# Kernel tuning notes

Hardware: AMD Instinct MI355X
Metric: run time of the kernel (lower is better)

Reference implementation:

```python
import jax, jax.numpy as jnp
import numpy as np

EPS = 1e-5

def _bn(x, g, b):
    # eval-mode BatchNorm2d with running_mean=0, running_var=1
    return x * (g / jnp.sqrt(1.0 + EPS))[None, :, None, None] + b[None, :, None, None]

def _dwconv2d(x, w, kh, kw, ph, pw):
    C = x.shape[1]
    k = w.reshape(C, 1, kh, kw)
    return jax.lax.conv_general_dilated(x, k, (1, 1), [(ph, ph), (pw, pw)],
                                        dimension_numbers=('NCHW', 'OIHW', 'NCHW'),
                                        feature_group_count=C)

def _mamba_seq(x, ln_g, ln_b, in_w, conv_w, conv_b, xproj_w, dt_w, dt_b, A_log, Dp, out_w):
    # x: (B, L, C) -> LayerNorm -> Mamba block (mamba-ssm math)
    B, L, C = x.shape
    di = conv_w.shape[0]; ds = A_log.shape[1]; dtr = dt_w.shape[1]; dc = conv_w.shape[1]
    mu = x.mean(-1, keepdims=True)
    var = ((x - mu) ** 2).mean(-1, keepdims=True)
    xn = (x - mu) / jnp.sqrt(var + EPS) * ln_g + ln_b
    xz = xn @ in_w.T                      # (B, L, 2*di)
    xm, z = xz[..., :di], xz[..., di:]
    # causal depthwise conv1d along L
    xc = xm.transpose(0, 2, 1)            # (B, di, L)
    k = conv_w.reshape(di, 1, dc)
    xc = jax.lax.conv_general_dilated(xc, k, (1,), [(dc - 1, 0)],
                                      dimension_numbers=('NCH', 'OIH', 'NCH'),
                                      feature_group_count=di)
    xm = jax.nn.silu((xc + conv_b[None, :, None]).transpose(0, 2, 1))  # (B, L, di)
    proj = xm @ xproj_w.T                 # (B, L, dtr + 2*ds)
    dt = jax.nn.softplus(proj[..., :dtr] @ dt_w.T + dt_b)              # (B, L, di)
    Bm = proj[..., dtr:dtr + ds]          # (B, L, ds)
    Cm = proj[..., dtr + ds:]             # (B, L, ds)
    A = -jnp.exp(A_log)                   # (di, ds)
    dA = jnp.exp(dt[..., None] * A)                       # (B, L, di, ds)
    dBx = (dt * xm)[..., None] * Bm[:, :, None, :]        # (B, L, di, ds)

    def step(h, inp):
        dA_t, dBx_t, C_t = inp
        h = dA_t * h + dBx_t
        y = jnp.einsum('bds,bs->bd', h, C_t)
        return h, y

    h0 = jnp.zeros((B, di, ds), x.dtype)
    xs = (dA.transpose(1, 0, 2, 3), dBx.transpose(1, 0, 2, 3), Cm.transpose(1, 0, 2))
    _, ys = jax.lax.scan(step, h0, xs)
    y = ys.transpose(1, 0, 2) + Dp * xm
    y = y * jax.nn.silu(z)
    return y @ out_w.T

def _mamba2d(x, *mp):
    B, C, H, W = x.shape
    s = x.reshape(B, C, H * W).transpose(0, 2, 1)
    s = _mamba_seq(s, *mp)
    return s.transpose(0, 2, 1).reshape(B, C, H, W)

def _forward(x, reduce_w, bn0_g, bn0_b, proj_w, bn1_g, bn1_b, dwh_w, bnh_g, bnh_b,
             dwv_w, bnv_g, bnv_b, fus_w, fus_b, ln_g, ln_b, in_w, conv_w, conv_b,
             xproj_w, dt_w, dt_b, A_log, Dp, out_w, fc1_w, fc2_w):
    C = reduce_w.shape[0]
    x = jax.nn.relu(_bn(jnp.einsum('bchw,oc->bohw', x, reduce_w), bn0_g, bn0_b))
    # local branch: StripConvBlock (depthwise strips)
    p = jax.nn.relu(_bn(jnp.einsum('bchw,oc->bohw', x, proj_w), bn1_g, bn1_b))
    h = jax.nn.relu(_bn(_dwconv2d(p, dwh_w, 1, 7, 0, 3), bnh_g, bnh_b))
    v = jax.nn.relu(_bn(_dwconv2d(p, dwv_w, 7, 1, 3, 0), bnv_g, bnv_b))
    feat_local = jnp.einsum('bchw,oc->bohw', h + v, fus_w) + fus_b[None, :, None, None]
    # global branch: 4-directional shared-weight Mamba
    mp = (ln_g, ln_b, in_w, conv_w, conv_b, xproj_w, dt_w, dt_b, A_log, Dp, out_w)
    x1 = _mamba2d(x, *mp)
    x2 = _mamba2d(x[:, :, ::-1, ::-1], *mp)[:, :, ::-1, ::-1]
    xt = x.swapaxes(2, 3)
    x3 = _mamba2d(xt, *mp).swapaxes(2, 3)
    x4 = _mamba2d(xt[:, :, ::-1, ::-1], *mp)[:, :, ::-1, ::-1].swapaxes(2, 3)
    feat_global = (x1 + x2 + x3 + x4) / 4.0 + x
    # SK fusion
    U = feat_local + feat_global
    s = U.mean((2, 3))                                   # (B, C)
    zf = jax.nn.relu(s @ fc1_w.T) @ fc2_w.T              # (B, 2C)
    w = jax.nn.softmax(zf.reshape(-1, 2, C), axis=1)
    return w[:, 0, :, None, None] * feat_local + w[:, 1, :, None, None] * feat_global

def setup_inputs() -> dict:
    key = jax.random.key(0)
    ks = jax.random.split(key, 16)
    B, Cin, C, H, W = 2, 512, 256, 48, 48
    di, ds, dtr, dc, mid = 512, 16, 16, 4, 16
    n = lambda i, shape, s=0.05: jax.random.normal(ks[i], shape, jnp.float32) * s
    return {
        'x': n(0, (B, Cin, H, W), 1.0),
        'reduce_w': n(1, (C, Cin)),
        'bn0_g': jnp.ones(C), 'bn0_b': jnp.zeros(C),
        'proj_w': n(2, (C, C)),
        'bn1_g': jnp.ones(C), 'bn1_b': jnp.zeros(C),
        'dwh_w': n(3, (C, 7), 0.2), 'bnh_g': jnp.ones(C), 'bnh_b': jnp.zeros(C),
        'dwv_w': n(4, (C, 7), 0.2), 'bnv_g': jnp.ones(C), 'bnv_b': jnp.zeros(C),
        'fus_w': n(5, (C, C)), 'fus_b': jnp.zeros(C),
        'ln_g': jnp.ones(C), 'ln_b': jnp.zeros(C),
        'in_w': n(6, (2 * di, C)),
        'conv_w': n(7, (di, dc), 0.2), 'conv_b': jnp.zeros(di),
        'xproj_w': n(8, (dtr + 2 * ds, di)),
        'dt_w': n(9, (di, dtr)), 'dt_b': jnp.full((di,), -4.0, jnp.float32),
        'A_log': jnp.tile(jnp.log(jnp.arange(1, ds + 1, dtype=jnp.float32)), (di, 1)),
        'Dp': jnp.ones(di),
        'out_w': n(10, (C, di)),
        'fc1_w': n(11, (mid, C)), 'fc2_w': n(12, (2 * C, mid)),
    }

def reference(x, reduce_w, bn0_g, bn0_b, proj_w, bn1_g, bn1_b, dwh_w, bnh_g, bnh_b,
              dwv_w, bnv_g, bnv_b, fus_w, fus_b, ln_g, ln_b, in_w, conv_w, conv_b,
              xproj_w, dt_w, dt_b, A_log, Dp, out_w, fc1_w, fc2_w):
    return _forward(x, reduce_w, bn0_g, bn0_b, proj_w, bn1_g, bn1_b, dwh_w, bnh_g, bnh_b,
                    dwv_w, bnv_g, bnv_b, fus_w, fus_b, ln_g, ln_b, in_w, conv_w, conv_b,
                    xproj_w, dt_w, dt_b, A_log, Dp, out_w, fc1_w, fc2_w)
```

## Files before the change

kernel.cpp:

```cpp
#include <hip/hip_runtime.h>
#include <hip/hip_bf16.h>

#define EPSC 1e-5f
#define Bn 2
#define CIN 512
#define Cc 256
#define Hh 48
#define Ww 48
#define Ll 2304
#define DI 512
#define DS 16
#define DTR 16
#define MROWS (Bn * Ll)
#define NCHUNK 8
#define CLEN (Ll / NCHUNK)
#define CTILES (CLEN / 32)

using bf16 = __hip_bfloat16;
typedef short v8s __attribute__((ext_vector_type(8)));
typedef float v4f __attribute__((ext_vector_type(4)));

__device__ __forceinline__ float ldIn(const void* p, size_t i, bool bf) {
    return bf ? __bfloat162float(((const bf16*)p)[i]) : ((const float*)p)[i];
}
__device__ __forceinline__ float toF(float v) { return v; }
__device__ __forceinline__ float toF(bf16 v) { return __bfloat162float(v); }
__device__ __forceinline__ void stO(float* p, float v) { *p = v; }
__device__ __forceinline__ void stO(bf16* p, float v) { *p = __float2bfloat16(v); }
__device__ __forceinline__ float bfu2f(unsigned short u) {
    return __uint_as_float(((unsigned int)u) << 16);
}
__device__ __forceinline__ short f2bs(float f) {
    bf16 h = __float2bfloat16(f);
    short s;
    __builtin_memcpy(&s, &h, 2);
    return s;
}
union U16B { uint4 u; v8s v; };
__device__ __forceinline__ v8s ldA8(const bf16* p) { U16B t; t.u = *(const uint4*)p; return t.v; }
__device__ __forceinline__ v8s ldW8(const void* W, size_t idx, bool bf) {
    if (bf) return ldA8((const bf16*)W + idx);
    const float* f = (const float*)W + idx;
    float4 a = *(const float4*)f;
    float4 b = *(const float4*)(f + 4);
    v8s r;
    r[0] = f2bs(a.x); r[1] = f2bs(a.y); r[2] = f2bs(a.z); r[3] = f2bs(a.w);
    r[4] = f2bs(b.x); r[5] = f2bs(b.y); r[6] = f2bs(b.z); r[7] = f2bs(b.w);
    return r;
}

__device__ __forceinline__ int perm_rt(int dir, int t) {
    if (dir == 0) return t;
    if (dir == 1) return Ll - 1 - t;
    int tt = (dir == 2) ? t : (Ll - 1 - t);
    int h = tt % Hh, w = tt / Hh;
    return h * Ww + w;
}

__global__ void k_detect(const unsigned int* __restrict__ xb, int* __restrict__ flag) {
    if (threadIdx.x == 0 && blockIdx.x == 0) {
        int cnt = 0;
        for (int i = 0; i < 64; i++) {
            unsigned int u = xb[i];
            unsigned int lo = u & 0xFFFFu;
            int e = (int)((lo >> 7) & 0xFF);
            if (lo == 0u || (e >= 90 && e <= 160)) cnt++;
        }
        *flag = (cnt >= 60) ? 1 : 0;
    }
}

__global__ __launch_bounds__(256) void k_probe(bf16* __restrict__ out, int n, float val) {
    int i = blockIdx.x * 256 + threadIdx.x;
    if (i < n) out[i] = __float2bfloat16(val);
}

__global__ __launch_bounds__(256) void k_transpose_in(const void* __restrict__ x, bf16* __restrict__ xT,
                                                      const int* __restrict__ dflag) {
    bool bf = (*dflag != 0);
    __shared__ float tile[32][33];
    int b = blockIdx.z;
    int l0 = blockIdx.x * 32, c0 = blockIdx.y * 32;
    int tx = threadIdx.x, ty = threadIdx.y;
    #pragma unroll
    for (int i = 0; i < 4; i++) {
        int c = c0 + ty + i * 8;
        tile[ty + i * 8][tx] = ldIn(x, ((size_t)(b * CIN + c)) * Ll + l0 + tx, bf);
    }
    __syncthreads();
    #pragma unroll
    for (int i = 0; i < 4; i++) {
        int l = l0 + ty + i * 8;
        xT[((size_t)(b * Ll + l)) * CIN + c0 + tx] = __float2bfloat16(tile[tx][ty + i * 8]);
    }
}

template <int EP, int KT, typename TO>
__global__ __launch_bounds__(256) void k_mgemm(const bf16* __restrict__ A, const void* __restrict__ W,
                                               TO* __restrict__ Out, int M, int N,
                                               const void* __restrict__ g, const void* __restrict__ bias,
                                               const int* __restrict__ dflag) {
    bool bf = (*dflag != 0);
    constexpr int K = KT * 32;
    int tid = threadIdx.x;
    int w = tid >> 6, lane = tid & 63, quad = lane >> 4, lm = lane & 15;
    int m_w = blockIdx.y * 128 + w * 32;
    int n_w = blockIdx.x * 64;
    v4f acc[2][4] = {};
    const bf16* aP0 = A + (size_t)(m_w + lm) * K + quad * 8;
    const bf16* aP1 = A + (size_t)(m_w + 16 + lm) * K + quad * 8;
    size_t wIdx[4];
    #pragma unroll
    for (int ni = 0; ni < 4; ni++) {
        int n = n_w + ni * 16 + lm;
        wIdx[ni] = (size_t)((n < N) ? n : 0) * K + quad * 8;
    }
    for (int kt = 0; kt < KT; kt++) {
        v8s a0 = ldA8(aP0 + kt * 32);
        v8s a1 = ldA8(aP1 + kt * 32);
        v8s bfr[4];
        #pragma unroll
        for (int ni = 0; ni < 4; ni++) bfr[ni] = ldW8(W, wIdx[ni] + kt * 32, bf);
        #pragma unroll
        for (int ni = 0; ni < 4; ni++) {
            acc[0][ni] = __builtin_amdgcn_mfma_f32_16x16x32_bf16(a0, bfr[ni], acc[0][ni], 0, 0, 0);
            acc[1][ni] = __builtin_amdgcn_mfma_f32_16x16x32_bf16(a1, bfr[ni], acc[1][ni], 0, 0, 0);
        }
    }
    float rs = rsqrtf(1.f + EPSC);
    #pragma unroll
    for (int mi = 0; mi < 2; mi++) {
        #pragma unroll
        for (int ni = 0; ni < 4; ni++) {
            int col = n_w + ni * 16 + lm;
            if (col >= N) continue;
            float gv = 0.f, bv = 0.f;
            if (EP == 1) { gv = ldIn(g, col, bf) * rs; bv = ldIn(bias, col, bf); }
            if (EP == 2) { bv = ldIn(bias, col, bf); }
            #pragma unroll
            for (int r = 0; r < 4; r++) {
                int row = m_w + mi * 16 + quad * 4 + r;
                float v = acc[mi][ni][r];
                if (EP == 1) v = fmaxf(v * gv + bv, 0.f);
                else if (EP == 2) v += bv;
                stO(&Out[(size_t)row * N + col], v);
            }
        }
    }
}

__global__ __launch_bounds__(256) void k_outgemm(const bf16* __restrict__ Y, const void* __restrict__ W,
                                                 const bf16* __restrict__ xrb, float* __restrict__ fg,
                                                 const int* __restrict__ dflag) {
    bool bf = (*dflag != 0);
    int tid = threadIdx.x;
    int w = tid >> 6, lane = tid & 63, quad = lane >> 4, lm = lane & 15;
    int row0 = blockIdx.y * 128 + w * 32;
    int n_w = blockIdx.x * 64;
    int b = row0 / Ll;
    v4f acc[2][4] = {};
    const bf16* aP[4][2];
    #pragma unroll
    for (int mi = 0; mi < 2; mi++) {
        int l = (row0 + mi * 16 + lm) - b * Ll;
        int h = l / Ww, w2 = l % Ww;
        int t2 = w2 * Hh + h;
        int tArr[4] = { l, Ll - 1 - l, t2, Ll - 1 - t2 };
        #pragma unroll
        for (int dir = 0; dir < 4; dir++)
            aP[dir][mi] = Y + ((size_t)dir * MROWS + (size_t)b * Ll + tArr[dir]) * DI + quad * 8;
    }
    size_t wIdx[4];
    #pragma unroll
    for (int ni = 0; ni < 4; ni++) wIdx[ni] = (size_t)(n_w + ni * 16 + lm) * DI + quad * 8;
    for (int kt = 0; kt < 16; kt++) {
        v8s bfr[4];
        #pragma unroll
        for (int ni = 0; ni < 4; ni++) bfr[ni] = ldW8(W, wIdx[ni] + kt * 32, bf);
        #pragma unroll
        for (int dir = 0; dir < 4; dir++) {
            v8s a0 = ldA8(aP[dir][0] + kt * 32);
            v8s a1 = ldA8(aP[dir][1] + kt * 32);
            #pragma unroll
            for (int ni = 0; ni < 4; ni++) {
                acc[0][ni] = __builtin_amdgcn_mfma_f32_16x16x32_bf16(a0, bfr[ni], acc[0][ni], 0, 0, 0);
                acc[1][ni] = __builtin_amdgcn_mfma_f32_16x16x32_bf16(a1, bfr[ni], acc[1][ni], 0, 0, 0);
            }
        }
    }
    #pragma unroll
    for (int mi = 0; mi < 2; mi++) {
        #pragma unroll
        for (int ni = 0; ni < 4; ni++) {
            int col = n_w + ni * 16 + lm;
            #pragma unroll
            for (int r = 0; r < 4; r++) {
                int row = row0 + mi * 16 + quad * 4 + r;
                size_t off = (size_t)row * Cc + col;
                fg[off] = toF(xrb[off]) + 0.25f * acc[mi][ni][r];
            }
        }
    }
}

__global__ __launch_bounds__(256) void k_ln(const bf16* __restrict__ xrb, const void* __restrict__ g,
                                            const void* __restrict__ bvec, bf16* __restrict__ xn,
                                            const int* __restrict__ dflag) {
    bool bf = (*dflag != 0);
    int m = blockIdx.x;
    int c = threadIdx.x;
    float v = toF(xrb[(size_t)m * Cc + c]);
    float s1 = v, s2 = v * v;
    #pragma unroll
    for (int off = 32; off; off >>= 1) {
        s1 += __shfl_down(s1, off);
        s2 += __shfl_down(s2, off);
    }
    __shared__ float a1[4], a2[4];
    int w = c >> 6;
    if ((c & 63) == 0) { a1[w] = s1; a2[w] = s2; }
    __syncthreads();
    float t1 = a1[0] + a1[1] + a1[2] + a1[3];
    float t2 = a2[0] + a2[1] + a2[2] + a2[3];
    float mu = t1 * (1.f / 256.f);
    float var = t2 * (1.f / 256.f) - mu * mu;
    float r = rsqrtf(var + EPSC);
    xn[(size_t)m * Cc + c] = __float2bfloat16((v - mu) * r * ldIn(g, c, bf) + ldIn(bvec, c, bf));
}

__global__ __launch_bounds__(256) void k_dwconv_hv(const bf16* __restrict__ p, const void* __restrict__ dwh,
                                                   const void* __restrict__ bnhg, const void* __restrict__ bnhb,
                                                   const void* __restrict__ dwv, const void* __restrict__ bnvg,
                                                   const void* __restrict__ bnvb, bf16* __restrict__ hv,
                                                   const int* __restrict__ dflag) {
    bool bf = (*dflag != 0);
    int m = blockIdx.x;
    int c = threadIdx.x;
    int b = m / Ll, l = m % Ll;
    int yy = l / Ww, xx = l % Ww;
    const bf16* base = p + (size_t)b * Ll * Cc;
    float ah = 0.f, av = 0.f;
    #pragma unroll
    for (int j = 0; j < 7; j++) {
        int x2 = xx + j - 3;
        if (0 <= x2 && x2 < Ww) ah += ldIn(dwh, c * 7 + j, bf) * toF(base[(size_t)(yy * Ww + x2) * Cc + c]);
        int y2 = yy + j - 3;
        if (0 <= y2 && y2 < Hh) av += ldIn(dwv, c * 7 + j, bf) * toF(base[(size_t)(y2 * Ww + xx) * Cc + c]);
    }
    float rs = rsqrtf(1.f + EPSC);
    float out = fmaxf(ah * ldIn(bnhg, c, bf) * rs + ldIn(bnhb, c, bf), 0.f) +
                fmaxf(av * ldIn(bnvg, c, bf) * rs + ldIn(bnvb, c, bf), 0.f);
    hv[(size_t)m * Cc + c] = __float2bfloat16(out);
}

__global__ __launch_bounds__(512) void k_conv1d(const bf16* __restrict__ xz, const void* __restrict__ cw,
                                                const void* __restrict__ cb, bf16* __restrict__ xm2,
                                                const int* __restrict__ dflag) {
    bool bf = (*dflag != 0);
    int m = blockIdx.x;
    int dir = blockIdx.y;
    int ch = threadIdx.x;
    int b = m / Ll, t = m % Ll;
    float acc = ldIn(cb, ch, bf);
    #pragma unroll
    for (int j = 0; j < 4; j++) {
        int tt = t + j - 3;
        if (tt >= 0) {
            int l = perm_rt(dir, tt);
            acc += ldIn(cw, ch * 4 + j, bf) * __bfloat162float(xz[((size_t)(b * Ll + l)) * 1024 + ch]);
        }
    }
    xm2[((size_t)dir * MROWS + m) * DI + ch] = __float2bfloat16(acc / (1.f + __expf(-acc)));
}

__global__ __launch_bounds__(256) void k_scanA(const bf16* __restrict__ xm2y, const float* __restrict__ proj4,
                                               float* __restrict__ hfin, float* __restrict__ sumdt,
                                               const void* __restrict__ A_log, const void* __restrict__ dt_w,
                                               const void* __restrict__ dt_b, const int* __restrict__ dflag) {
    bool bf = (*dflag != 0);
    int tid = threadIdx.x;
    int w = tid >> 6, lane = tid & 63;
    int g = lane >> 4, s = lane & 15;
    int c = blockIdx.x % 56;
    int j32 = blockIdx.x / 56;
    int chunk = c >> 3;
    int dir = (c & 7) >> 1;
    int b = c & 1;
    int jj = j32 * 4 + w;
    int ch0 = jj * 4;
    int ch = ch0 + g;

    float Acoef = -__expf(ldIn(A_log, ch * 16 + s, bf));
    float dtbias = ldIn(dt_b, ch, bf);
    float dtwv[16];
    #pragma unroll
    for (int r = 0; r < 16; r++) dtwv[r] = ldIn(dt_w, ch * DTR + r, bf);
    float h = 0.f, sacc = 0.f;

    __shared__ float sP[2][32 * 33];
    __shared__ uint2 sxm[4][32];
    __shared__ float sdt[4][128];

    const bf16* xmS = xm2y + ((size_t)dir * MROWS + (size_t)b * Ll) * DI;
    const float* ppS = proj4 + ((size_t)dir * MROWS + (size_t)b * Ll) * 48;
    int t0c = chunk * CLEN;
    int ttl = lane & 31;
    bool isA = lane < 32;

    float rp[4];
    ushort4 rxm;
    #pragma unroll
    for (int k = 0; k < 4; k++) {
        int idx = tid + k * 256;
        int t = idx >> 5, r = idx & 31;
        sP[0][t * 33 + r] = ppS[(size_t)(t0c + t) * 48 + r];
    }
    if (isA) {
        rxm = *(const ushort4*)(xmS + (size_t)(t0c + ttl) * DI + ch0);
        sxm[w][ttl] = *(uint2*)&rxm;
    }
    __syncthreads();

    int buf = 0;
    for (int tile = 0; tile < CTILES; tile++) {
        if (tile < CTILES - 1) {
            int tb = t0c + (tile + 1) * 32;
            #pragma unroll
            for (int k = 0; k < 4; k++) {
                int idx = tid + k * 256;
                int t = idx >> 5, r = idx & 31;
                rp[k] = ppS[(size_t)(tb + t) * 48 + r];
            }
            if (isA) rxm = *(const ushort4*)(xmS + (size_t)(tb + ttl) * DI + ch0);
        }
        const float* P = sP[buf];
        const unsigned short* xml = (const unsigned short*)sxm[w];
        {
            float d0 = dtbias, d1 = dtbias;
            #pragma unroll
            for (int r = 0; r < 16; r++) {
                float wv = dtwv[r];
                d0 = fmaf(P[s * 33 + r], wv, d0);
                d1 = fmaf(P[(16 + s) * 33 + r], wv, d1);
            }
            d0 = (d0 > 20.f) ? d0 : __logf(1.f + __expf(d0));
            d1 = (d1 > 20.f) ? d1 : __logf(1.f + __expf(d1));
            sdt[w][s * 4 + g] = d0;
            sdt[w][(16 + s) * 4 + g] = d1;
        }
        #pragma unroll
        for (int half = 0; half < 2; half++) {
            float da[16], uu[16];
            #pragma unroll
            for (int q = 0; q < 16; q++) {
                int tt = half * 16 + q;
                float dtv = sdt[w][tt * 4 + g];
                float xv = bfu2f(xml[tt * 4 + g]);
                float Bv = P[tt * 33 + 16 + s];
                da[q] = __expf(dtv * Acoef);
                uu[q] = dtv * xv * Bv;
                sacc += dtv;
            }
            #pragma unroll
            for (int q = 0; q < 16; q++) h = fmaf(da[q], h, uu[q]);
        }
        if (tile < CTILES - 1) {
            int nb = buf ^ 1;
            #pragma unroll
            for (int k = 0; k < 4; k++) {
                int idx = tid + k * 256;
                int t = idx >> 5, r = idx & 31;
                sP[nb][t * 33 + r] = rp[k];
            }
            if (isA) sxm[w][ttl] = *(uint2*)&rxm;
            __syncthreads();
            buf = nb;
        }
    }
    int db = (dir * 2 + b);
    hfin[(((size_t)db * NCHUNK + chunk) << 13) + ch * 16 + s] = h;
    if (s == 0) sumdt[(((size_t)db * NCHUNK + chunk) << 9) + ch] = sacc * 0.0625f * 16.f;
}

__global__ __launch_bounds__(256) void k_scanB(float* __restrict__ hfin, const float* __restrict__ sumdt,
                                               const void* __restrict__ A_log, const int* __restrict__ dflag) {
    bool bf = (*dflag != 0);
    int idx = blockIdx.x * 256 + threadIdx.x;
    int s = idx & 15, ch = (idx >> 4) & 511;
    int db = idx >> 13;
    float Acoef = -__expf(ldIn(A_log, ch * 16 + s, bf));
    float h = 0.f;
    size_t base = ((size_t)db * NCHUNK << 13) + ch * 16 + s;
    size_t sbase = ((size_t)db * NCHUNK << 9) + ch;
    #pragma unroll
    for (int k = 0; k < NCHUNK; k++) {
        float hf = hfin[base + ((size_t)k << 13)];
        hfin[base + ((size_t)k << 13)] = h;
        if (k < NCHUNK - 1) {
            float a = __expf(Acoef * sumdt[sbase + ((size_t)k << 9)]);
            h = a * h + hf;
        }
    }
}

__global__ __launch_bounds__(256) void k_scanC(bf16* __restrict__ xm2y, const float* __restrict__ proj4,
                                               const bf16* __restrict__ xz, const float* __restrict__ hfin,
                                               const void* __restrict__ A_log, const void* __restrict__ Dp,
                                               const void* __restrict__ dt_w, const void* __restrict__ dt_b,
                                               const int* __restrict__ dflag) {
    bool bf = (*dflag != 0);
    int tid = threadIdx.x;
    int w = tid >> 6, lane = tid & 63;
    int g = lane >> 4, s = lane & 15;
    int c = blockIdx.x & 63;
    int j32 = blockIdx.x >> 6;
    int chunk = c >> 3;
    int dir = (c & 7) >> 1;
    int b = c & 1;
    int jj = j32 * 4 + w;
    int ch0 = jj * 4;
    int ch = ch0 + g;

    float Acoef = -__expf(ldIn(A_log, ch * 16 + s, bf));
    float dp = ldIn(Dp, ch, bf);
    float dtbias = ldIn(dt_b, ch, bf);
    float dtwv[16];
    #pragma unroll
    for (int r = 0; r < 16; r++) dtwv[r] = ldIn(dt_w, ch * DTR + r, bf);
    int db = (dir * 2 + b);
    float h = hfin[(((size_t)db * NCHUNK + chunk) << 13) + ch * 16 + s];

    __shared__ float sP[2][32 * 49];
    __shared__ uint2 sxm[4][32];
    __shared__ uint2 szz[4][32];
    __shared__ float sdt[4][128];

    bf16* xmS = xm2y + ((size_t)dir * MROWS + (size_t)b * Ll) * DI;
    const float* ppS = proj4 + ((size_t)dir * MROWS + (size_t)b * Ll) * 48;
    const bf16* zp = xz + (size_t)b * Ll * 1024 + 512;
    int t0c = chunk * CLEN;
    int ttl = lane & 31;
    bool isA = lane < 32;

    float rp[6];
    ushort4 rxz;
    #pragma unroll
    for (int k = 0; k < 6; k++) {
        int idx = tid + k * 256;
        int t = idx / 48, r = idx % 48;
        sP[0][t * 49 + r] = ppS[(size_t)(t0c + t) * 48 + r];
    }
    if (isA) {
        rxz = *(const ushort4*)(xmS + (size_t)(t0c + ttl) * DI + ch0);
        sxm[w][ttl] = *(uint2*)&rxz;
    } else {
        int l = perm_rt(dir, t0c + ttl);
        rxz = *(const ushort4*)(zp + (size_t)l * 1024 + ch0);
        szz[w][ttl] = *(uint2*)&rxz;
    }
    __syncthreads();

    int buf = 0;
    for (int tile = 0; tile < CTILES; tile++) {
        if (tile < CTILES - 1) {
            int tb = t0c + (tile + 1) * 32;
            #pragma unroll
            for (int k = 0; k < 6; k++) {
                int idx = tid + k * 256;
                int t = idx / 48, r = idx % 48;
                rp[k] = ppS[(size_t)(tb + t) * 48 + r];
            }
            if (isA) rxz = *(const ushort4*)(xmS + (size_t)(tb + ttl) * DI + ch0);
            else {
                int l = perm_rt(dir, tb + ttl);
                rxz = *(const ushort4*)(zp + (size_t)l * 1024 + ch0);
            }
        }
        const float* P = sP[buf];
        const unsigned short* xml = (const unsigned short*)sxm[w];
        const unsigned short* zl  = (const unsigned short*)szz[w];
        int tbase = t0c + tile * 32;
        {
            float d0 = dtbias, d1 = dtbias;
            #pragma unroll
            for (int r = 0; r < 16; r++) {
                float wv = dtwv[r];
                d0 = fmaf(P[s * 49 + r], wv, d0);
                d1 = fmaf(P[(16 + s) * 49 + r], wv, d1);
            }
            d0 = (d0 > 20.f) ? d0 : __logf(1.f + __expf(d0));
            d1 = (d1 > 20.f) ? d1 : __logf(1.f + __expf(d1));
            sdt[w][s * 4 + g] = d0;
            sdt[w][(16 + s) * 4 + g] = d1;
        }
        float pc[32];
        #pragma unroll
        for (int half = 0; half < 2; half++) {
            float da[16], uu[16];
            #pragma unroll
            for (int q = 0; q < 16; q++) {
                int tt = half * 16 + q;
                float dtv = sdt[w][tt * 4 + g];
                float xv = bfu2f(xml[tt * 4 + g]);
                float Bv = P[tt * 49 + 16 + s];
                da[q] = __expf(dtv * Acoef);
                uu[q] = dtv * xv * Bv;
            }
            #pragma unroll
            for (int q = 0; q < 16; q++) {
                int tt = half * 16 + q;
                h = fmaf(da[q], h, uu[q]);
                pc[tt] = h * P[tt * 49 + 32 + s];
            }
        }
        #pragma unroll
        for (int r = 8; r; r >>= 1) {
            #pragma unroll
            for (int tt = 0; tt < 32; tt++) pc[tt] += __shfl_xor(pc[tt], r);
        }
        #pragma unroll
        for (int k = 0; k < 2; k++) {
            int tt = s + 16 * k;
            float xv = bfu2f(xml[tt * 4 + g]);
            float zv = bfu2f(zl[tt * 4 + g]);
            float sig = 1.f / (1.f + __expf(-zv));
            xmS[(size_t)(tbase + tt) * DI + ch] = __float2bfloat16((pc[tt] + dp * xv) * zv * sig);
        }
        if (tile < CTILES - 1) {
            int nb = buf ^ 1;
            #pragma unroll
            for (int k = 0; k < 6; k++) {
                int idx = tid + k * 256;
                int t = idx / 48, r = idx % 48;
                sP[nb][t * 49 + r] = rp[k];
            }
            if (isA) sxm[w][ttl] = *(uint2*)&rxz;
            else szz[w][ttl] = *(uint2*)&rxz;
            __syncthreads();
            buf = nb;
        }
    }
}

__global__ __launch_bounds__(256) void k_meanU(const bf16* __restrict__ fl, const float* __restrict__ fg,
                                               float* __restrict__ ssum) {
    int b = blockIdx.y;
    int chunk = blockIdx.x;
    int c = threadIdx.x;
    float acc = 0.f;
    for (int i = 0; i < 72; i++) {
        int l = chunk * 72 + i;
        size_t off = ((size_t)(b * Ll + l)) * Cc + c;
        acc += toF(fl[off]) + fg[off];
    }
    atomicAdd(&ssum[b * Cc + c], acc);
}

__global__ __launch_bounds__(256) void k_se(const float* __restrict__ ssum, const void* __restrict__ fc1,
                                            const void* __restrict__ fc2, float* __restrict__ w01,
                                            const int* __restrict__ dflag) {
    bool bf = (*dflag != 0);
    int b = blockIdx.x;
    int c = threadIdx.x;
    __shared__ float sh[256];
    __shared__ float mid[16];
    sh[c] = ssum[b * 256 + c] * (1.f / (float)Ll);
    __syncthreads();
    if (c < 16) {
        float a = 0.f;
        for (int k = 0; k < 256; k++) a += sh[k] * ldIn(fc1, c * 256 + k, bf);
        mid[c] = fmaxf(a, 0.f);
    }
    __syncthreads();
    float a0 = 0.f, a1 = 0.f;
    #pragma unroll
    for (int j = 0; j < 16; j++) {
        float mj = mid[j];
        a0 += mj * ldIn(fc2, c * 16 + j, bf);
        a1 += mj * ldIn(fc2, (256 + c) * 16 + j, bf);
    }
    float mx = fmaxf(a0, a1);
    float e0 = expf(a0 - mx), e1 = expf(a1 - mx);
    float inv = 1.f / (e0 + e1);
    w01[b * 256 + c] = e0 * inv;
    w01[512 + b * 256 + c] = e1 * inv;
}

__global__ __launch_bounds__(256) void k_final(const bf16* __restrict__ fl, const float* __restrict__ fg,
                                               const float* __restrict__ w01, void* __restrict__ out,
                                               const int* __restrict__ dflag) {
    bool bf = (*dflag != 0);
    __shared__ float tile[32][33];
    int b = blockIdx.z;
    int l0 = blockIdx.x * 32, c0 = blockIdx.y * 32;
    int tx = threadIdx.x, ty = threadIdx.y;
    #pragma unroll
    for (int i = 0; i < 4; i++) {
        int l = l0 + ty + i * 8;
        int c = c0 + tx;
        size_t off = ((size_t)(b * Ll + l)) * Cc + c;
        tile[ty + i * 8][tx] = w01[b * 256 + c] * toF(fl[off]) + w01[512 + b * 256 + c] * fg[off];
    }
    __syncthreads();
    #pragma unroll
    for (int i = 0; i < 4; i++) {
        int c = c0 + ty + i * 8;
        size_t off = ((size_t)(b * Cc + c)) * Ll + l0 + tx;
        float v = tile[tx][ty + i * 8];
        if (bf) ((bf16*)out)[off] = __float2bfloat16(v);
        else    ((float*)out)[off] = v;
    }
}

extern "C" void kernel_launch(void* const* d_in, const int* in_sizes, int n_in,
                              void* d_out, int out_size, void* d_ws, size_t ws_size,
                              hipStream_t stream) {
    const void* x        = d_in[0];
    const void* reduce_w = d_in[1];
    const void* bn0_g    = d_in[2];
    const void* bn0_b    = d_in[3];
    const void* proj_w   = d_in[4];
    const void* bn1_g    = d_in[5];
    const void* bn1_b    = d_in[6];
    const void* dwh_w    = d_in[7];
    const void* bnh_g    = d_in[8];
    const void* bnh_b    = d_in[9];
    const void* dwv_w    = d_in[10];
    const void* bnv_g    = d_in[11];
    const void* bnv_b    = d_in[12];
    const void* fus_w    = d_in[13];
    const void* fus_b    = d_in[14];
    const void* ln_g     = d_in[15];
    const void* ln_b     = d_in[16];
    const void* in_w     = d_in[17];
    const void* conv_w   = d_in[18];
    const void* conv_b   = d_in[19];
    const void* xproj_w  = d_in[20];
    const void* dt_w     = d_in[21];
    const void* dt_b     = d_in[22];
    const void* A_log    = d_in[23];
    const void* Dp       = d_in[24];
    const void* out_w    = d_in[25];
    const void* fc1_w    = d_in[26];
    const void* fc2_w    = d_in[27];

    float* ws = (float*)d_ws;
    bf16*  fl     = (bf16*)ws;
    float* fg     = ws + 589824;
    bf16*  xrb    = (bf16*)(ws + 1769472);
    bf16*  xz     = (bf16*)(ws + 2359296);
    float* proj4  = ws + 4718592;
    bf16*  xm2y   = (bf16*)(ws + 5603328);
    float* scrH   = ws + 10321920;
    float* ssum   = ws + 10911744;
    float* w01    = ws + 10912256;
    int*   dflag  = (int*)(ws + 10913280);
    const size_t needed = 10913281ULL * 4ULL;

    if (ws_size < needed) {
        float val = 1000.0f + (float)(ws_size >> 20);
        k_probe<<<(out_size + 255) / 256, 256, 0, stream>>>((bf16*)d_out, out_size, val);
        return;
    }

    bf16* xTb = (bf16*)xm2y;
    bf16* hvb = (bf16*)xm2y;
    bf16* pb  = (bf16*)scrH;
    bf16* xnb = (bf16*)scrH;
    float* hfin  = scrH;
    float* sumdt = scrH + 524288;

    k_detect<<<1, 64, 0, stream>>>((const unsigned int*)x, dflag);
    k_transpose_in<<<dim3(Ll / 32, CIN / 32, Bn), dim3(32, 8), 0, stream>>>(x, xTb, dflag);
    k_mgemm<1, 16, bf16><<<dim3(4, MROWS / 128), 256, 0, stream>>>(xTb, reduce_w, xrb, MROWS, Cc, bn0_g, bn0_b, dflag);
    k_mgemm<1, 8, bf16><<<dim3(4, MROWS / 128), 256, 0, stream>>>(xrb, proj_w, pb, MROWS, Cc, bn1_g, bn1_b, dflag);
    k_dwconv_hv<<<MROWS, 256, 0, stream>>>(pb, dwh_w, bnh_g, bnh_b, dwv_w, bnv_g, bnv_b, hvb, dflag);
    k_mgemm<2, 8, bf16><<<dim3(4, MROWS / 128), 256, 0, stream>>>(hvb, fus_w, fl, MROWS, Cc, nullptr, fus_b, dflag);
    k_ln<<<MROWS, 256, 0, stream>>>(xrb, ln_g, ln_b, xnb, dflag);
    k_mgemm<0, 8, bf16><<<dim3(16, MROWS / 128), 256, 0, stream>>>(xnb, in_w, xz, MROWS, 2 * DI, nullptr, nullptr, dflag);
    k_conv1d<<<dim3(MROWS, 4), 512, 0, stream>>>(xz, conv_w, conv_b, xm2y, dflag);
    k_mgemm<0, 16, float><<<dim3(1, 4 * MROWS / 128), 256, 0, stream>>>(xm2y, xproj_w, proj4, 4 * MROWS, DTR + 2 * DS, nullptr, nullptr, dflag);
    k_scanA<<<(NCHUNK - 1) * 256, 256, 0, stream>>>(xm2y, proj4, hfin, sumdt, A_log, dt_w, dt_b, dflag);
    k_scanB<<<256, 256, 0, stream>>>(hfin, sumdt, A_log, dflag);
    k_scanC<<<NCHUNK * 256, 256, 0, stream>>>(xm2y, proj4, xz, hfin, A_log, Dp, dt_w, dt_b, dflag);
    k_outgemm<<<dim3(4, MROWS / 128), 256, 0, stream>>>(xm2y, out_w, xrb, fg, dflag);
    hipMemsetAsync(ssum, 0, 512 * 4, stream);
    k_meanU<<<dim3(32, Bn), 256, 0, stream>>>(fl, fg, ssum);
    k_se<<<Bn, 256, 0, stream>>>(ssum, fc1_w, fc2_w, w01, dflag);
    k_final<<<dim3(Ll / 32, Cc / 32, Bn), dim3(32, 8), 0, stream>>>(fl, fg, w01, d_out, dflag);
}
```

Measured before the change: 594.9 us.

## Halve GEMM row tiles, fuse LayerNorm into in-proj GEMM, use more scan chunks

The GEMM kernels now give each wave 16 rows instead of 32, which doubles the number of blocks and raises occupancy for this small problem. The cost is that each loaded weight fragment is reused across fewer rows. LayerNorm is folded into the in-projection GEMM, which computes row statistics from register-held A fragments, so the separate LN kernel and its intermediate buffer go away. The chunked scan goes from 8 to 12 chunks for more parallelism, at the price of a longer sequential scanB and more carry state in the workspace.

```diff
diff --git a/kernel.cpp b/kernel.cpp
--- a/kernel.cpp
+++ b/kernel.cpp
@@ -12,7 +12,7 @@
 #define DS 16
 #define DTR 16
 #define MROWS (Bn * Ll)
-#define NCHUNK 8
+#define NCHUNK 12
 #define CLEN (Ll / NCHUNK)
 #define CTILES (CLEN / 32)
 
@@ -104,11 +104,10 @@
     constexpr int K = KT * 32;
     int tid = threadIdx.x;
     int w = tid >> 6, lane = tid & 63, quad = lane >> 4, lm = lane & 15;
-    int m_w = blockIdx.y * 128 + w * 32;
+    int m_w = blockIdx.y * 64 + w * 16;
     int n_w = blockIdx.x * 64;
-    v4f acc[2][4] = {};
-    const bf16* aP0 = A + (size_t)(m_w + lm) * K + quad * 8;
-    const bf16* aP1 = A + (size_t)(m_w + 16 + lm) * K + quad * 8;
+    v4f acc[4] = {};
+    const bf16* aP = A + (size_t)(m_w + lm) * K + quad * 8;
     size_t wIdx[4];
     #pragma unroll
     for (int ni = 0; ni < 4; ni++) {
@@ -116,35 +115,91 @@
         wIdx[ni] = (size_t)((n < N) ? n : 0) * K + quad * 8;
     }
     for (int kt = 0; kt < KT; kt++) {
-        v8s a0 = ldA8(aP0 + kt * 32);
-        v8s a1 = ldA8(aP1 + kt * 32);
+        v8s a0 = ldA8(aP + kt * 32);
         v8s bfr[4];
         #pragma unroll
         for (int ni = 0; ni < 4; ni++) bfr[ni] = ldW8(W, wIdx[ni] + kt * 32, bf);
         #pragma unroll
-        for (int ni = 0; ni < 4; ni++) {
-            acc[0][ni] = __builtin_amdgcn_mfma_f32_16x16x32_bf16(a0, bfr[ni], acc[0][ni], 0, 0, 0);
-            acc[1][ni] = __builtin_amdgcn_mfma_f32_16x16x32_bf16(a1, bfr[ni], acc[1][ni], 0, 0, 0);
-        }
+        for (int ni = 0; ni < 4; ni++)
+            acc[ni] = __builtin_amdgcn_mfma_f32_16x16x32_bf16(a0, bfr[ni], acc[ni], 0, 0, 0);
     }
     float rs = rsqrtf(1.f + EPSC);
     #pragma unroll
-    for (int mi = 0; mi < 2; mi++) {
-        #pragma unroll
-        for (int ni = 0; ni < 4; ni++) {
-            int col = n_w + ni * 16 + lm;
-            if (col >= N) continue;
-            float gv = 0.f, bv = 0.f;
-            if (EP == 1) { gv = ldIn(g, col, bf) * rs; bv = ldIn(bias, col, bf); }
-            if (EP == 2) { bv = ldIn(bias, col, bf); }
-            #pragma unroll
-            for (int r = 0; r < 4; r++) {
-                int row = m_w + mi * 16 + quad * 4 + r;
-                float v = acc[mi][ni][r];
-                if (EP == 1) v = fmaxf(v * gv + bv, 0.f);
-                else if (EP == 2) v += bv;
-                stO(&Out[(size_t)row * N + col], v);
-            }
+    for (int ni = 0; ni < 4; ni++) {
+        int col = n_w + ni * 16 + lm;
+        if (col >= N) continue;
+        float gv = 0.f, bv = 0.f;
+        if (EP == 1) { gv = ldIn(g, col, bf) * rs; bv = ldIn(bias, col, bf); }
+        if (EP == 2) { bv = ldIn(bias, col, bf); }
+        #pragma unroll
+        for (int r = 0; r < 4; r++) {
+            int row = m_w + quad * 4 + r;
+            float v = acc[ni][r];
+            if (EP == 1) v = fmaxf(v * gv + bv, 0.f);
+            else if (EP == 2) v += bv;
+            stO(&Out[(size_t)row * N + col], v);
+        }
+    }
+}
+
+__global__ __launch_bounds__(256) void k_lngemm(const bf16* __restrict__ A, const void* __restrict__ W,
+                                                bf16* __restrict__ Out, const void* __restrict__ lng,
+                                                const void* __restrict__ lnb, const int* __restrict__ dflag) {
+    bool bf = (*dflag != 0);
+    constexpr int KT = 8, K = 256, N = 2 * DI;
+    int tid = threadIdx.x;
+    int w = tid >> 6, lane = tid & 63, quad = lane >> 4, lm = lane & 15;
+    int m_w = blockIdx.y * 64 + w * 16;
+    int n_w = blockIdx.x * 64;
+    __shared__ float sg[256], sb[256];
+    sg[tid] = ldIn(lng, tid, bf);
+    sb[tid] = ldIn(lnb, tid, bf);
+    __syncthreads();
+    const bf16* aP = A + (size_t)(m_w + lm) * K + quad * 8;
+    v8s araw[8];
+    float s1 = 0.f, s2 = 0.f;
+    #pragma unroll
+    for (int kt = 0; kt < KT; kt++) {
+        araw[kt] = ldA8(aP + kt * 32);
+        #pragma unroll
+        for (int e = 0; e < 8; e++) {
+            float v = bfu2f((unsigned short)araw[kt][e]);
+            s1 += v; s2 += v * v;
+        }
+    }
+    s1 += __shfl_xor(s1, 16); s2 += __shfl_xor(s2, 16);
+    s1 += __shfl_xor(s1, 32); s2 += __shfl_xor(s2, 32);
+    float mu = s1 * (1.f / 256.f);
+    float var = s2 * (1.f / 256.f) - mu * mu;
+    float r = rsqrtf(var + EPSC);
+    #pragma unroll
+    for (int kt = 0; kt < KT; kt++) {
+        #pragma unroll
+        for (int e = 0; e < 8; e++) {
+            int c = kt * 32 + quad * 8 + e;
+            float v = bfu2f((unsigned short)araw[kt][e]);
+            araw[kt][e] = f2bs((v - mu) * r * sg[c] + sb[c]);
+        }
+    }
+    v4f acc[4] = {};
+    size_t wIdx[4];
+    #pragma unroll
+    for (int ni = 0; ni < 4; ni++) wIdx[ni] = (size_t)(n_w + ni * 16 + lm) * K + quad * 8;
+    for (int kt = 0; kt < KT; kt++) {
+        v8s bfr[4];
+        #pragma unroll
+        for (int ni = 0; ni < 4; ni++) bfr[ni] = ldW8(W, wIdx[ni] + kt * 32, bf);
+        #pragma unroll
+        for (int ni = 0; ni < 4; ni++)
+            acc[ni] = __builtin_amdgcn_mfma_f32_16x16x32_bf16(araw[kt], bfr[ni], acc[ni], 0, 0, 0);
+    }
+    #pragma unroll
+    for (int ni = 0; ni < 4; ni++) {
+        int col = n_w + ni * 16 + lm;
+        #pragma unroll
+        for (int r2 = 0; r2 < 4; r2++) {
+            int row = m_w + quad * 4 + r2;
+            Out[(size_t)row * N + col] = __float2bfloat16(acc[ni][r2]);
         }
     }
 }
@@ -155,20 +210,19 @@
     bool bf = (*dflag != 0);
     int tid = threadIdx.x;
     int w = tid >> 6, lane = tid & 63, quad = lane >> 4, lm = lane & 15;
-    int row0 = blockIdx.y * 128 + w * 32;
+    int row0 = blockIdx.y * 64 + w * 16;
     int n_w = blockIdx.x * 64;
     int b = row0 / Ll;
-    v4f acc[2][4] = {};
-    const bf16* aP[4][2];
-    #pragma unroll
-    for (int mi = 0; mi < 2; mi++) {
-        int l = (row0 + mi * 16 + lm) - b * Ll;
+    v4f acc[4] = {};
+    const bf16* aP[4];
+    {
+        int l = (row0 + lm) - b * Ll;
         int h = l / Ww, w2 = l % Ww;
         int t2 = w2 * Hh + h;
         int tArr[4] = { l, Ll - 1 - l, t2, Ll - 1 - t2 };
         #pragma unroll
         for (int dir = 0; dir < 4; dir++)
-            aP[dir][mi] = Y + ((size_t)dir * MROWS + (size_t)b * Ll + tArr[dir]) * DI + quad * 8;
+            aP[dir] = Y + ((size_t)dir * MROWS + (size_t)b * Ll + tArr[dir]) * DI + quad * 8;
     }
     size_t wIdx[4];
     #pragma unroll
@@ -179,53 +233,22 @@
         for (int ni = 0; ni < 4; ni++) bfr[ni] = ldW8(W, wIdx[ni] + kt * 32, bf);
         #pragma unroll
         for (int dir = 0; dir < 4; dir++) {
-            v8s a0 = ldA8(aP[dir][0] + kt * 32);
-            v8s a1 = ldA8(aP[dir][1] + kt * 32);
-            #pragma unroll
-            for (int ni = 0; ni < 4; ni++) {
-                acc[0][ni] = __builtin_amdgcn_mfma_f32_16x16x32_bf16(a0, bfr[ni], acc[0][ni], 0, 0, 0);
-                acc[1][ni] = __builtin_amdgcn_mfma_f32_16x16x32_bf16(a1, bfr[ni], acc[1][ni], 0, 0, 0);
-            }
-        }
-    }
-    #pragma unroll
-    for (int mi = 0; mi < 2; mi++) {
-        #pragma unroll
-        for (int ni = 0; ni < 4; ni++) {
-            int col = n_w + ni * 16 + lm;
-            #pragma unroll
-            for (int r = 0; r < 4; r++) {
-                int row = row0 + mi * 16 + quad * 4 + r;
-                size_t off = (size_t)row * Cc + col;
-                fg[off] = toF(xrb[off]) + 0.25f * acc[mi][ni][r];
-            }
-        }
-    }
-}
-
-__global__ __launch_bounds__(256) void k_ln(const bf16* __restrict__ xrb, const void* __restrict__ g,
-                                            const void* __restrict__ bvec, bf16* __restrict__ xn,
-                                            const int* __restrict__ dflag) {
-    bool bf = (*dflag != 0);
-    int m = blockIdx.x;
-    int c = threadIdx.x;
-    float v = toF(xrb[(size_t)m * Cc + c]);
-    float s1 = v, s2 = v * v;
-    #pragma unroll
-    for (int off = 32; off; off >>= 1) {
-        s1 += __shfl_down(s1, off);
-        s2 += __shfl_down(s2, off);
-    }
-    __shared__ float a1[4], a2[4];
-    int w = c >> 6;
-    if ((c & 63) == 0) { a1[w] = s1; a2[w] = s2; }
-    __syncthreads();
-    float t1 = a1[0] + a1[1] + a1[2] + a1[3];
-    float t2 = a2[0] + a2[1] + a2[2] + a2[3];
-    float mu = t1 * (1.f / 256.f);
-    float var = t2 * (1.f / 256.f) - mu * mu;
-    float r = rsqrtf(var + EPSC);
-    xn[(size_t)m * Cc + c] = __float2bfloat16((v - mu) * r * ldIn(g, c, bf) + ldIn(bvec, c, bf));
+            v8s a0 = ldA8(aP[dir] + kt * 32);
+            #pragma unroll
+            for (int ni = 0; ni < 4; ni++)
+                acc[ni] = __builtin_amdgcn_mfma_f32_16x16x32_bf16(a0, bfr[ni], acc[ni], 0, 0, 0);
+        }
+    }
+    #pragma unroll
+    for (int ni = 0; ni < 4; ni++) {
+        int col = n_w + ni * 16 + lm;
+        #pragma unroll
+        for (int r = 0; r < 4; r++) {
+            int row = row0 + quad * 4 + r;
+            size_t off = (size_t)row * Cc + col;
+            fg[off] = toF(xrb[off]) + 0.25f * acc[ni][r];
+        }
+    }
 }
 
 __global__ __launch_bounds__(256) void k_dwconv_hv(const bf16* __restrict__ p, const void* __restrict__ dwh,
@@ -281,8 +304,9 @@
     int tid = threadIdx.x;
     int w = tid >> 6, lane = tid & 63;
     int g = lane >> 4, s = lane & 15;
-    int c = blockIdx.x % 56;
-    int j32 = blockIdx.x / 56;
+    const int NCOMBO = (NCHUNK - 1) * 8;
+    int c = blockIdx.x % NCOMBO;
+    int j32 = blockIdx.x / NCOMBO;
     int chunk = c >> 3;
     int dir = (c & 7) >> 1;
     int b = c & 1;
@@ -379,7 +403,7 @@
     }
     int db = (dir * 2 + b);
     hfin[(((size_t)db * NCHUNK + chunk) << 13) + ch * 16 + s] = h;
-    if (s == 0) sumdt[(((size_t)db * NCHUNK + chunk) << 9) + ch] = sacc * 0.0625f * 16.f;
+    if (s == 0) sumdt[(((size_t)db * NCHUNK + chunk) << 9) + ch] = sacc;
 }
 
 __global__ __launch_bounds__(256) void k_scanB(float* __restrict__ hfin, const float* __restrict__ sumdt,
@@ -412,8 +436,9 @@
     int tid = threadIdx.x;
     int w = tid >> 6, lane = tid & 63;
     int g = lane >> 4, s = lane & 15;
-    int c = blockIdx.x & 63;
-    int j32 = blockIdx.x >> 6;
+    const int NCOMBO = NCHUNK * 8;
+    int c = blockIdx.x % NCOMBO;
+    int j32 = blockIdx.x / NCOMBO;
     int chunk = c >> 3;
     int dir = (c & 7) >> 1;
     int b = c & 1;
@@ -652,10 +677,10 @@
     float* proj4  = ws + 4718592;
     bf16*  xm2y   = (bf16*)(ws + 5603328);
     float* scrH   = ws + 10321920;
-    float* ssum   = ws + 10911744;
-    float* w01    = ws + 10912256;
-    int*   dflag  = (int*)(ws + 10913280);
-    const size_t needed = 10913281ULL * 4ULL;
+    float* ssum   = ws + 11157504;
+    float* w01    = ws + 11158016;
+    int*   dflag  = (int*)(ws + 11159040);
+    const size_t needed = 11159041ULL * 4ULL;
 
     if (ws_size < needed) {
         float val = 1000.0f + (float)(ws_size >> 20);
@@ -666,24 +691,22 @@
     bf16* xTb = (bf16*)xm2y;
     bf16* hvb = (bf16*)xm2y;
     bf16* pb  = (bf16*)scrH;
-    bf16* xnb = (bf16*)scrH;
     float* hfin  = scrH;
-    float* sumdt = scrH + 524288;
+    float* sumdt = scrH + 786432;
 
     k_detect<<<1, 64, 0, stream>>>((const unsigned int*)x, dflag);
     k_transpose_in<<<dim3(Ll / 32, CIN / 32, Bn), dim3(32, 8), 0, stream>>>(x, xTb, dflag);
-    k_mgemm<1, 16, bf16><<<dim3(4, MROWS / 128), 256, 0, stream>>>(xTb, reduce_w, xrb, MROWS, Cc, bn0_g, bn0_b, dflag);
-    k_mgemm<1, 8, bf16><<<dim3(4, MROWS / 128), 256, 0, stream>>>(xrb, proj_w, pb, MROWS, Cc, bn1_g, bn1_b, dflag);
+    k_mgemm<1, 16, bf16><<<dim3(4, MROWS / 64), 256, 0, stream>>>(xTb, reduce_w, xrb, MROWS, Cc, bn0_g, bn0_b, dflag);
+    k_mgemm<1, 8, bf16><<<dim3(4, MROWS / 64), 256, 0, stream>>>(xrb, proj_w, pb, MROWS, Cc, bn1_g, bn1_b, dflag);
     k_dwconv_hv<<<MROWS, 256, 0, stream>>>(pb, dwh_w, bnh_g, bnh_b, dwv_w, bnv_g, bnv_b, hvb, dflag);
-    k_mgemm<2, 8, bf16><<<dim3(4, MROWS / 128), 256, 0, stream>>>(hvb, fus_w, fl, MROWS, Cc, nullptr, fus_b, dflag);
-    k_ln<<<MROWS, 256, 0, stream>>>(xrb, ln_g, ln_b, xnb, dflag);
-    k_mgemm<0, 8, bf16><<<dim3(16, MROWS / 128), 256, 0, stream>>>(xnb, in_w, xz, MROWS, 2 * DI, nullptr, nullptr, dflag);
+    k_mgemm<2, 8, bf16><<<dim3(4, MROWS / 64), 256, 0, stream>>>(hvb, fus_w, fl, MROWS, Cc, nullptr, fus_b, dflag);
+    k_lngemm<<<dim3(16, MROWS / 64), 256, 0, stream>>>(xrb, in_w, xz, ln_g, ln_b, dflag);
     k_conv1d<<<dim3(MROWS, 4), 512, 0, stream>>>(xz, conv_w, conv_b, xm2y, dflag);
-    k_mgemm<0, 16, float><<<dim3(1, 4 * MROWS / 128), 256, 0, stream>>>(xm2y, xproj_w, proj4, 4 * MROWS, DTR + 2 * DS, nullptr, nullptr, dflag);
-    k_scanA<<<(NCHUNK - 1) * 256, 256, 0, stream>>>(xm2y, proj4, hfin, sumdt, A_log, dt_w, dt_b, dflag);
+    k_mgemm<0, 16, float><<<dim3(1, 4 * MROWS / 64), 256, 0, stream>>>(xm2y, xproj_w, proj4, 4 * MROWS, DTR + 2 * DS, nullptr, nullptr, dflag);
+    k_scanA<<<(NCHUNK - 1) * 8 * 32, 256, 0, stream>>>(xm2y, proj4, hfin, sumdt, A_log, dt_w, dt_b, dflag);
     k_scanB<<<256, 256, 0, stream>>>(hfin, sumdt, A_log, dflag);
-    k_scanC<<<NCHUNK * 256, 256, 0, stream>>>(xm2y, proj4, xz, hfin, A_log, Dp, dt_w, dt_b, dflag);
-    k_outgemm<<<dim3(4, MROWS / 128), 256, 0, stream>>>(xm2y, out_w, xrb, fg, dflag);
+    k_scanC<<<NCHUNK * 8 * 32, 256, 0, stream>>>(xm2y, proj4, xz, hfin, A_log, Dp, dt_w, dt_b, dflag);
+    k_outgemm<<<dim3(4, MROWS / 64), 256, 0, stream>>>(xm2y, out_w, xrb, fg, dflag);
     hipMemsetAsync(ssum, 0, 512 * 4, stream);
     k_meanU<<<dim3(32, Bn), 256, 0, stream>>>(fl, fg, ssum);
     k_se<<<Bn, 256, 0, stream>>>(ssum, fc1_w, fc2_w, w01, dflag);
```

After: 670.9 us. 12.8% more time.
